# Kernel optimization log

Hardware: AMD Instinct MI355X
Metric: run time of the kernel (lower is better)

The kernel has to match this reference:

```python
import jax, jax.numpy as jnp
import numpy as np

N = 50000
E = 800000
IN_DIM = 128
OUT_DIM = 64


def setup_inputs() -> dict:
    key = jax.random.key(0)
    ks = jax.random.split(key, 6)
    adj = jax.random.randint(ks[0], (2, E), 0, N)
    h = jax.random.normal(ks[1], (N, IN_DIM), dtype=jnp.float32)
    # fc: Linear(in_dim, out_dim) -> weight [out_dim, in_dim], bias [out_dim]
    W_fc = jax.random.normal(ks[2], (OUT_DIM, IN_DIM), dtype=jnp.float32) * (1.0 / np.sqrt(IN_DIM))
    b_fc = jnp.zeros((OUT_DIM,), dtype=jnp.float32)
    # attn_fc: Linear(2*out_dim, 1) -> weight [1, 2*out_dim], bias [1]
    W_att = jax.random.normal(ks[3], (1, 2 * OUT_DIM), dtype=jnp.float32) * (1.0 / np.sqrt(2 * OUT_DIM))
    b_att = jnp.zeros((1,), dtype=jnp.float32)
    return {"adj": adj, "h": h, "W_fc": W_fc, "b_fc": b_fc, "W_att": W_att, "b_att": b_att}


def reference(adj, h, W_fc, b_fc, W_att, b_att):
    # z = fc(h): [N, out_dim]
    z = h @ W_fc.T + b_fc
    src = adj[0]
    dst = adj[1]
    z_src = z[src]  # [E, out_dim]
    z_dst = z[dst]  # [E, out_dim]
    # attn_fc(cat(z_src, z_dst)) == z_src @ W1 + z_dst @ W2 + b; avoid explicit concat split
    w1 = W_att[0, :OUT_DIM]
    w2 = W_att[0, OUT_DIM:]
    att_logit = z_src @ w1 + z_dst @ w2 + b_att[0]  # [E]
    att_edge = jax.nn.leaky_relu(att_logit, negative_slope=0.01)[:, None]  # [E, 1]
    # scatter-add weighted source features to destination nodes
    out = jax.ops.segment_sum(z_src * att_edge, dst, num_segments=N)  # [N, out_dim]
    return out
```

## Files before the change

kernel.cpp:

```cpp
#include <hip/hip_runtime.h>
#include <hip/hip_bf16.h>

#define N_NODES 50000
#define E_EDGES 800000
#define IN_DIM  128
#define OUT_DIM 64
#define MTILES  (N_NODES / 16)
#define NB      196
#define BCAP    6144
#define OVF_CAP 16384
#define NBLK_FC 782
#define NBLK_SA 256
#define EPA     3125

static_assert(N_NODES % 16 == 0, "16-row MFMA tiles");
static_assert(N_NODES < 65536, "node ids packed in 16 bits");
static_assert(NBLK_SA * EPA == E_EDGES, "pass-A blocks partition edges");
static_assert(NB * 256 >= N_NODES, "buckets cover dst space");


typedef __attribute__((ext_vector_type(8))) short bf16x8;
typedef __attribute__((ext_vector_type(4))) float f32x4;
typedef __attribute__((ext_vector_type(8))) unsigned short u16x8;

__device__ __forceinline__ unsigned short f32_to_bf16_rne(float f) {
    unsigned u = __float_as_uint(f);
    return (unsigned short)((u + 0x7FFFu + ((u >> 16) & 1u)) >> 16);
}
__device__ __forceinline__ float bf16_to_f32(unsigned short s) {
    return __uint_as_float(((unsigned)s) << 16);
}

__global__ __launch_bounds__(256) void gat_fc_scatter(
    const float* __restrict__ h,
    const float* __restrict__ Wfc,
    const float* __restrict__ bfc,
    const float* __restrict__ Watt,
    const float* __restrict__ batt,
    const int*   __restrict__ adj,
    unsigned short* __restrict__ z16,
    float* __restrict__ s1,
    float* __restrict__ s2,
    int*      __restrict__ gcnt,
    unsigned* __restrict__ coarse,
    unsigned* __restrict__ ovf)
{
    __shared__ short Wlds[OUT_DIM][IN_DIM + 8];

    if (blockIdx.x < NBLK_FC) {
        for (int i = threadIdx.x; i < OUT_DIM * IN_DIM; i += 256) {
            const int o = i >> 7;
            const int k = i & 127;
            Wlds[o][k] = (short)f32_to_bf16_rne(Wfc[i]);
        }
        __syncthreads();

        const int lane  = threadIdx.x & 63;
        const int c     = lane & 15;
        const int q     = lane >> 4;
        const int mtile = blockIdx.x * 4 + (threadIdx.x >> 6);
        if (mtile >= MTILES) return;
        const int n0 = mtile * 16;

        bf16x8 B[4][4];
        #pragma unroll
        for (int t = 0; t < 4; ++t)
            #pragma unroll
            for (int f = 0; f < 4; ++f)
                B[t][f] = *(const bf16x8*)&Wlds[f * 16 + c][t * 32 + q * 8];

        f32x4 acc[4] = {{0,0,0,0},{0,0,0,0},{0,0,0,0},{0,0,0,0}};

        const float* arow = h + (size_t)(n0 + c) * IN_DIM + q * 8;
        #pragma unroll
        for (int t = 0; t < 4; ++t) {
            float4 x0 = *(const float4*)(arow + t * 32);
            float4 x1 = *(const float4*)(arow + t * 32 + 4);
            bf16x8 a;
            a[0] = (short)f32_to_bf16_rne(x0.x);
            a[1] = (short)f32_to_bf16_rne(x0.y);
            a[2] = (short)f32_to_bf16_rne(x0.z);
            a[3] = (short)f32_to_bf16_rne(x0.w);
            a[4] = (short)f32_to_bf16_rne(x1.x);
            a[5] = (short)f32_to_bf16_rne(x1.y);
            a[6] = (short)f32_to_bf16_rne(x1.z);
            a[7] = (short)f32_to_bf16_rne(x1.w);
            #pragma unroll
            for (int f = 0; f < 4; ++f)
                acc[f] = __builtin_amdgcn_mfma_f32_16x16x32_bf16(a, B[t][f], acc[f], 0, 0, 0);
        }

        const float batt0 = batt[0];
        float w1c[4], w2c[4], bv[4];
        #pragma unroll
        for (int f = 0; f < 4; ++f) {
            w1c[f] = Watt[f * 16 + c];
            w2c[f] = Watt[OUT_DIM + f * 16 + c];
            bv[f]  = bfc[f * 16 + c];
        }
        float p1[4] = {0,0,0,0}, p2[4] = {0,0,0,0};
        #pragma unroll
        for (int f = 0; f < 4; ++f)
            #pragma unroll
            for (int r = 0; r < 4; ++r) {
                const float v = acc[f][r] + bv[f];
                z16[(size_t)(n0 + q * 4 + r) * OUT_DIM + f * 16 + c] = f32_to_bf16_rne(v);
                p1[r] += v * w1c[f];
                p2[r] += v * w2c[f];
            }
        #pragma unroll
        for (int r = 0; r < 4; ++r) {
            #pragma unroll
            for (int off = 1; off < 16; off <<= 1) {
                p1[r] += __shfl_xor(p1[r], off, 64);
                p2[r] += __shfl_xor(p2[r], off, 64);
            }
            if (c == 0) {
                s1[n0 + q * 4 + r] = p1[r];
                s2[n0 + q * 4 + r] = p2[r] + batt0;
            }
        }
    } else {
        __shared__ unsigned el[EPA];
        __shared__ int sof[256];
        __shared__ int bexc[NB], lcur[NB], gbase[NB];

        const int k  = blockIdx.x - NBLK_FC;
        const int e0 = k * EPA;
        const int t  = threadIdx.x;

        sof[t] = 0;
        __syncthreads();

        for (int i = t; i < EPA; i += 256)
            atomicAdd(&sof[adj[E_EDGES + e0 + i] >> 8], 1);
        __syncthreads();
        const int v = sof[t];
        __syncthreads();

        sof[t] = v;
        __syncthreads();
        #pragma unroll
        for (int o = 1; o < 256; o <<= 1) {
            const int add = (t >= o) ? sof[t - o] : 0;
            __syncthreads();
            sof[t] += add;
            __syncthreads();
        }
        if (t < NB) {
            const int excl = sof[t] - v;
            bexc[t]  = excl;
            lcur[t]  = excl;
            gbase[t] = atomicAdd(&gcnt[t], v);
        }
        __syncthreads();

        for (int i = t; i < EPA; i += 256) {
            const unsigned dst = (unsigned)adj[E_EDGES + e0 + i];
            const unsigned src = (unsigned)adj[e0 + i];
            const int b = (int)(dst >> 8);
            const int p = atomicAdd(&lcur[b], 1);
            el[p] = (dst << 16) | src;
        }
        __syncthreads();

        for (int i = t; i < EPA; i += 256) {
            const unsigned packed = el[i];
            const int b = (int)(packed >> 24);
            const int pin = gbase[b] + (i - bexc[b]);
            if (pin < BCAP) {
                coarse[(size_t)b * BCAP + pin] = packed;
            } else {
                const int o = atomicAdd(&gcnt[NB], 1);
                if (o < OVF_CAP) ovf[o] = packed;
            }
        }
    }
}

__global__ __launch_bounds__(256) void gat_binsort(
    unsigned* __restrict__ coarse,
    const int* __restrict__ gcnt,
    int* __restrict__ start, int* __restrict__ deg)
{
    __shared__ unsigned el[BCAP];
    __shared__ int hist[256], sof[256], cur[256];
    const int b  = blockIdx.x;
    const int t  = threadIdx.x;
    const int nb = min(gcnt[b], BCAP);

    for (int i = t; i < nb; i += 256) el[i] = coarse[(size_t)b * BCAP + i];
    hist[t] = 0;
    __syncthreads();

    for (int i = t; i < nb; i += 256)
        atomicAdd(&hist[(el[i] >> 16) & 255], 1);
    __syncthreads();

    const int v = hist[t];
    sof[t] = v;
    __syncthreads();
    #pragma unroll
    for (int o = 1; o < 256; o <<= 1) {
        const int add = (t >= o) ? sof[t - o] : 0;
        __syncthreads();
        sof[t] += add;
        __syncthreads();
    }
    const int excl = sof[t] - v;
    cur[t] = excl;
    const int n = b * 256 + t;
    if (n < N_NODES) {
        start[n] = b * BCAP + excl;
        deg[n]   = v;
    }
    __syncthreads();

    for (int i = t; i < nb; i += 256) {
        const unsigned e = el[i];
        const int p = atomicAdd(&cur[(e >> 16) & 255], 1);
        coarse[(size_t)b * BCAP + p] = e;
    }
}

__global__ __launch_bounds__(256) void gat_gather(
    const int* __restrict__ start, const int* __restrict__ deg,
    const unsigned* __restrict__ coarse, const int* __restrict__ gcnt,
    const unsigned* __restrict__ ovf,
    const float* __restrict__ s1, const float* __restrict__ s2,
    const unsigned short* __restrict__ z16,
    float* __restrict__ out)
{
    const int lane = threadIdx.x & 63;
    const int c    = lane & 7;
    const int q    = lane >> 3;
    const int n    = blockIdx.x * 4 + (threadIdx.x >> 6);
    if (n >= N_NODES) return;

    const int m  = deg[n];
    const int jb = start[n];
    const float s2n = s2[n];

    float acc[8] = {0,0,0,0,0,0,0,0};
    int j = 0;
    for (; j + 8 <= m; j += 8) {
        const int src = (int)(coarse[jb + j + q] & 0xFFFFu);
        float a = s1[src] + s2n;
        a = (a > 0.f) ? a : 0.01f * a;
        const u16x8 zz = *(const u16x8*)&z16[(size_t)src * OUT_DIM + 8 * c];
        #pragma unroll
        for (int t = 0; t < 8; ++t) acc[t] += a * bf16_to_f32(zz[t]);
    }
    if (q < m - j) {
        const int src = (int)(coarse[jb + j + q] & 0xFFFFu);
        float a = s1[src] + s2n;
        a = (a > 0.f) ? a : 0.01f * a;
        const u16x8 zz = *(const u16x8*)&z16[(size_t)src * OUT_DIM + 8 * c];
        #pragma unroll
        for (int t = 0; t < 8; ++t) acc[t] += a * bf16_to_f32(zz[t]);
    }

    const int novf = min(gcnt[NB], OVF_CAP);
    for (int base = 0; base < novf; base += 8) {
        const int idx = base + q;
        const unsigned packed = (idx < novf) ? ovf[idx] : 0xFFFFFFFFu;
        const bool valid = (idx < novf) && ((packed >> 16) == (unsigned)n);
        const int src = valid ? (int)(packed & 0xFFFFu) : 0;
        float a = s1[src] + s2n;
        a = (a > 0.f) ? a : 0.01f * a;
        a = valid ? a : 0.f;
        const u16x8 zz = *(const u16x8*)&z16[(size_t)src * OUT_DIM + 8 * c];
        #pragma unroll
        for (int t = 0; t < 8; ++t) acc[t] += a * bf16_to_f32(zz[t]);
    }

    #pragma unroll
    for (int t = 0; t < 8; ++t) {
        acc[t] += __shfl_xor(acc[t], 8, 64);
        acc[t] += __shfl_xor(acc[t], 16, 64);
        acc[t] += __shfl_xor(acc[t], 32, 64);
    }

    if (q == 0) {
        float4 lo = make_float4(acc[0], acc[1], acc[2], acc[3]);
        float4 hi = make_float4(acc[4], acc[5], acc[6], acc[7]);
        *(float4*)&out[(size_t)n * OUT_DIM + 8 * c]     = lo;
        *(float4*)&out[(size_t)n * OUT_DIM + 8 * c + 4] = hi;
    }
}

extern "C" void kernel_launch(void* const* d_in, const int* in_sizes, int n_in,
                              void* d_out, int out_size, void* d_ws, size_t ws_size,
                              hipStream_t stream)
{
    const int*   adj  = (const int*)  d_in[0];
    const float* h    = (const float*)d_in[1];
    const float* Wfc  = (const float*)d_in[2];
    const float* bfc  = (const float*)d_in[3];
    const float* Watt = (const float*)d_in[4];
    const float* batt = (const float*)d_in[5];
    float* out = (float*)d_out;

    unsigned short* z16 = (unsigned short*)d_ws;
    float* s1    = (float*)(z16 + (size_t)N_NODES * OUT_DIM);
    float* s2    = s1 + N_NODES;
    int*   start = (int*)(s2 + N_NODES);
    int*   deg   = start + N_NODES;
    int*   gcnt  = deg + N_NODES;
    unsigned* ovf    = (unsigned*)(gcnt + NB + 1);
    unsigned* coarse = ovf + OVF_CAP;

    hipMemsetAsync(gcnt, 0, (NB + 1) * sizeof(int), stream);

    gat_fc_scatter<<<NBLK_FC + NBLK_SA, 256, 0, stream>>>(
        h, Wfc, bfc, Watt, batt, adj, z16, s1, s2, gcnt, coarse, ovf);
    gat_binsort<<<NB, 256, 0, stream>>>(coarse, gcnt, start, deg);
    gat_gather<<<(N_NODES + 3) / 4, 256, 0, stream>>>(
        start, deg, coarse, gcnt, ovf, s1, s2, z16, out);
}
```

Measured before the change: 136.3 us.

## Rebalance scatter blocks, widen binsort, register-cache edges, unroll gather loop

Pass A now uses 625 blocks of 1280 edges each, and every thread loads its five dst/src pairs into registers once instead of reading adj twice. The binsort kernel moves to 512 threads and fuses the coarse load with the histogram. The gather kernel gains a 16-edge unrolled loop so two independent z rows are in flight per lane. Together these aim to cut repeated global loads and raise memory-level parallelism, at the cost of more global atomics on gcnt, more blocks and higher register use.

```diff
diff --git a/kernel.cpp b/kernel.cpp
--- a/kernel.cpp
+++ b/kernel.cpp
@@ -10,12 +10,14 @@
 #define BCAP    6144
 #define OVF_CAP 16384
 #define NBLK_FC 782
-#define NBLK_SA 256
-#define EPA     3125
+#define NBLK_SA 625
+#define EPA     1280
+#define ITER_A  5
 
 static_assert(N_NODES % 16 == 0, "16-row MFMA tiles");
 static_assert(N_NODES < 65536, "node ids packed in 16 bits");
 static_assert(NBLK_SA * EPA == E_EDGES, "pass-A blocks partition edges");
+static_assert(EPA == ITER_A * 256, "uniform per-thread trip count");
 static_assert(NB * 256 >= N_NODES, "buckets cover dst space");
 
 
@@ -132,8 +134,16 @@
         sof[t] = 0;
         __syncthreads();
 
-        for (int i = t; i < EPA; i += 256)
-            atomicAdd(&sof[adj[E_EDGES + e0 + i] >> 8], 1);
+        unsigned dv[ITER_A], sv[ITER_A];
+        #pragma unroll
+        for (int it = 0; it < ITER_A; ++it) {
+            dv[it] = (unsigned)adj[E_EDGES + e0 + t + it * 256];
+            sv[it] = (unsigned)adj[e0 + t + it * 256];
+        }
+
+        #pragma unroll
+        for (int it = 0; it < ITER_A; ++it)
+            atomicAdd(&sof[dv[it] >> 8], 1);
         __syncthreads();
         const int v = sof[t];
         __syncthreads();
@@ -155,16 +165,17 @@
         }
         __syncthreads();
 
-        for (int i = t; i < EPA; i += 256) {
-            const unsigned dst = (unsigned)adj[E_EDGES + e0 + i];
-            const unsigned src = (unsigned)adj[e0 + i];
-            const int b = (int)(dst >> 8);
+        #pragma unroll
+        for (int it = 0; it < ITER_A; ++it) {
+            const int b = (int)(dv[it] >> 8);
             const int p = atomicAdd(&lcur[b], 1);
-            el[p] = (dst << 16) | src;
-        }
-        __syncthreads();
-
-        for (int i = t; i < EPA; i += 256) {
+            el[p] = (dv[it] << 16) | sv[it];
+        }
+        __syncthreads();
+
+        #pragma unroll
+        for (int it = 0; it < ITER_A; ++it) {
+            const int i = t + it * 256;
             const unsigned packed = el[i];
             const int b = (int)(packed >> 24);
             const int pin = gbase[b] + (i - bexc[b]);
@@ -178,7 +189,7 @@
     }
 }
 
-__global__ __launch_bounds__(256) void gat_binsort(
+__global__ __launch_bounds__(512) void gat_binsort(
     unsigned* __restrict__ coarse,
     const int* __restrict__ gcnt,
     int* __restrict__ start, int* __restrict__ deg)
@@ -189,34 +200,40 @@
     const int t  = threadIdx.x;
     const int nb = min(gcnt[b], BCAP);
 
-    for (int i = t; i < nb; i += 256) el[i] = coarse[(size_t)b * BCAP + i];
-    hist[t] = 0;
+    if (t < 256) hist[t] = 0;
     __syncthreads();
 
-    for (int i = t; i < nb; i += 256)
-        atomicAdd(&hist[(el[i] >> 16) & 255], 1);
+    #pragma unroll 4
+    for (int i = t; i < nb; i += 512) {
+        const unsigned e = coarse[(size_t)b * BCAP + i];
+        el[i] = e;
+        atomicAdd(&hist[(e >> 16) & 255], 1);
+    }
     __syncthreads();
 
-    const int v = hist[t];
-    sof[t] = v;
+    const int v = (t < 256) ? hist[t] : 0;
+    if (t < 256) sof[t] = v;
     __syncthreads();
     #pragma unroll
     for (int o = 1; o < 256; o <<= 1) {
-        const int add = (t >= o) ? sof[t - o] : 0;
-        __syncthreads();
-        sof[t] += add;
-        __syncthreads();
-    }
-    const int excl = sof[t] - v;
-    cur[t] = excl;
-    const int n = b * 256 + t;
-    if (n < N_NODES) {
-        start[n] = b * BCAP + excl;
-        deg[n]   = v;
+        const int add = (t >= o && t < 256) ? sof[t - o] : 0;
+        __syncthreads();
+        if (t < 256) sof[t] += add;
+        __syncthreads();
+    }
+    if (t < 256) {
+        const int excl = sof[t] - v;
+        cur[t] = excl;
+        const int n = b * 256 + t;
+        if (n < N_NODES) {
+            start[n] = b * BCAP + excl;
+            deg[n]   = v;
+        }
     }
     __syncthreads();
 
-    for (int i = t; i < nb; i += 256) {
+    #pragma unroll 4
+    for (int i = t; i < nb; i += 512) {
         const unsigned e = el[i];
         const int p = atomicAdd(&cur[(e >> 16) & 255], 1);
         coarse[(size_t)b * BCAP + p] = e;
@@ -243,6 +260,20 @@
 
     float acc[8] = {0,0,0,0,0,0,0,0};
     int j = 0;
+    for (; j + 16 <= m; j += 16) {
+        const int srcA = (int)(coarse[jb + j + q] & 0xFFFFu);
+        const int srcB = (int)(coarse[jb + j + 8 + q] & 0xFFFFu);
+        float aA = s1[srcA] + s2n;
+        float aB = s1[srcB] + s2n;
+        aA = (aA > 0.f) ? aA : 0.01f * aA;
+        aB = (aB > 0.f) ? aB : 0.01f * aB;
+        const u16x8 zA = *(const u16x8*)&z16[(size_t)srcA * OUT_DIM + 8 * c];
+        const u16x8 zB = *(const u16x8*)&z16[(size_t)srcB * OUT_DIM + 8 * c];
+        #pragma unroll
+        for (int t = 0; t < 8; ++t) acc[t] += aA * bf16_to_f32(zA[t]);
+        #pragma unroll
+        for (int t = 0; t < 8; ++t) acc[t] += aB * bf16_to_f32(zB[t]);
+    }
     for (; j + 8 <= m; j += 8) {
         const int src = (int)(coarse[jb + j + q] & 0xFFFFu);
         float a = s1[src] + s2n;
@@ -314,7 +345,7 @@
 
     gat_fc_scatter<<<NBLK_FC + NBLK_SA, 256, 0, stream>>>(
         h, Wfc, bfc, Watt, batt, adj, z16, s1, s2, gcnt, coarse, ovf);
-    gat_binsort<<<NB, 256, 0, stream>>>(coarse, gcnt, start, deg);
+    gat_binsort<<<NB, 512, 0, stream>>>(coarse, gcnt, start, deg);
     gat_gather<<<(N_NODES + 3) / 4, 256, 0, stream>>>(
         start, deg, coarse, gcnt, ovf, s1, s2, z16, out);
 }
```

New measurement: 129.8 us. 4.7% less time.
